# Kernel optimization log

Hardware: AMD Instinct MI355X
Metric: run time of the kernel (lower is better)

Reference implementation:

```python
import jax, jax.numpy as jnp
import numpy as np

N = 100000
E = 1600000
D_IN = 128
D_HID = 128
EPS = 1e-5  # BatchNorm eps


def gcn_conv(x, edge_index, W, b, num_nodes):
    # PyG GCNConv: h = x @ W; symmetric norm with self-loops; out = scatter_add + b
    h = x @ W  # [N, D_out]
    loops = jnp.arange(num_nodes, dtype=edge_index.dtype)
    src = jnp.concatenate([edge_index[0], loops])
    dst = jnp.concatenate([edge_index[1], loops])
    ones = jnp.ones(src.shape[0], dtype=h.dtype)
    deg = jax.ops.segment_sum(ones, dst, num_segments=num_nodes)  # in-degree incl. self-loop
    dinv = jnp.where(deg > 0, jax.lax.rsqrt(deg), 0.0)
    norm = dinv[src] * dinv[dst]  # [E+N]
    msg = h[src] * norm[:, None]  # [E+N, D_out]  (largest intermediate)
    out = jax.ops.segment_sum(msg, dst, num_segments=num_nodes)
    return out + b


def batchnorm(h, gamma, beta):
    # training-mode batch statistics over the node dimension (biased variance)
    mean = jnp.mean(h, axis=0)
    var = jnp.mean(jnp.square(h - mean), axis=0)
    return (h - mean) * jax.lax.rsqrt(var + EPS) * gamma + beta


def setup_inputs() -> dict:
    key = jax.random.key(0)
    ks = jax.random.split(key, 8)
    x = jax.random.normal(ks[0], (N, D_IN), dtype=jnp.float32)
    edge_index = jax.random.randint(ks[1], (2, E), 0, N, dtype=jnp.int64)
    s1 = 1.0 / np.sqrt(D_IN)
    s2 = 1.0 / np.sqrt(D_HID)
    W1 = jax.random.uniform(ks[2], (D_IN, D_HID), jnp.float32, -s1, s1)
    b1 = jnp.zeros((D_HID,), jnp.float32)
    g1 = jnp.ones((D_HID,), jnp.float32)
    be1 = jnp.zeros((D_HID,), jnp.float32)
    W2 = jax.random.uniform(ks[3], (D_HID, D_HID), jnp.float32, -s2, s2)
    b2 = jnp.zeros((D_HID,), jnp.float32)
    g2 = jnp.ones((D_HID,), jnp.float32)
    be2 = jnp.zeros((D_HID,), jnp.float32)
    Wl = jax.random.uniform(ks[4], (D_HID, 1), jnp.float32, -s2, s2)
    bl = jax.random.uniform(ks[5], (1,), jnp.float32, -s2, s2)
    return {"x": x, "edge_index": edge_index, "W1": W1, "b1": b1, "g1": g1,
            "be1": be1, "W2": W2, "b2": b2, "g2": g2, "be2": be2,
            "Wl": Wl, "bl": bl}


def reference(x, edge_index, W1, b1, g1, be1, W2, b2, g2, be2, Wl, bl):
    h = gcn_conv(x, edge_index, W1, b1, N)
    h = jax.nn.relu(batchnorm(h, g1, be1))
    # dropout is identity in eval/deterministic reference
    h = gcn_conv(h, edge_index, W2, b2, N)
    h = jax.nn.relu(batchnorm(h, g2, be2))
    h = jax.nn.relu(h @ Wl + bl)  # [N, 1]
    return jax.nn.sigmoid(h)
```

## Files before the change

### kernel.cpp

```cpp
#include <hip/hip_runtime.h>
#include <cstdint>
#include <cstddef>

typedef unsigned int uint;
typedef unsigned short ushort;
typedef __attribute__((ext_vector_type(8))) short bf16x8;
typedef __attribute__((ext_vector_type(4))) float f32x4;

#define CAP 4608

__device__ __forceinline__ ushort f2bf(float f) {
    uint b = __float_as_uint(f);
    return (ushort)((b + 0x7FFF + ((b >> 16) & 1)) >> 16);
}
__device__ __forceinline__ float bf_lo(uint u) { return __uint_as_float(u << 16); }
__device__ __forceinline__ float bf_hi(uint u) { return __uint_as_float(u & 0xFFFF0000u); }

__global__ __launch_bounds__(512) void k_sort(
        const int* __restrict__ src, const int* __restrict__ dst, int E, int chunk,
        int* __restrict__ bcur, uint* __restrict__ ebuf, int nbkt,
        const float* __restrict__ W1, const float* __restrict__ W2,
        ushort* __restrict__ WT1, ushort* __restrict__ WT2,
        float* __restrict__ sums) {
    __shared__ uint   ebuf_l[8192];
    __shared__ ushort bid_l[8192];
    __shared__ int    sh[512];
    __shared__ int    hist[512], histx[512], cur[512], goff[512];
    const int t   = threadIdx.x;
    const int blk = blockIdx.x;

    {
        int wi = blk * 512 + t;
        if (wi < 16384) {
            int nn = wi >> 7, k = wi & 127;
            WT1[wi] = f2bf(W1[k * 128 + nn]);
        } else if (wi < 32768) {
            int wj = wi - 16384, nn = wj >> 7, k = wj & 127;
            WT2[wj] = f2bf(W2[k * 128 + nn]);
        } else if (wi < 36864) {
            sums[wi - 32768] = 0.f;
        }
    }

    hist[t] = 0;
    __syncthreads();

    const int beg = blk * chunk;
    const int end = min(beg + chunk, E);
    for (int i = beg + t; i < end; i += 512)
        atomicAdd(&hist[dst[i] >> 8], 1);
    __syncthreads();

    const int c = (t < nbkt) ? hist[t] : 0;
    sh[t] = c;
    __syncthreads();
    #pragma unroll
    for (int o = 1; o < 512; o <<= 1) {
        int x = (t >= o) ? sh[t - o] : 0;
        __syncthreads();
        sh[t] += x;
        __syncthreads();
    }
    const int ex = sh[t] - c;
    histx[t] = ex;
    cur[t]   = ex;
    {
        int base = (c > 0 && t < nbkt) ? atomicAdd(&bcur[t], c) : 0;
        goff[t] = t * CAP + base - ex;
    }
    __syncthreads();

    for (int i = beg + t; i < end; i += 512) {
        int d = dst[i];
        int s = src[i];
        int b = d >> 8;
        int p = atomicAdd(&cur[b], 1);
        ebuf_l[p] = ((uint)(d & 255) << 17) | (uint)s;
        bid_l[p]  = (ushort)b;
    }
    __syncthreads();

    const int cntE = end - beg;
    for (int i = t; i < cntE; i += 512)
        ebuf[goff[bid_l[i]] + i] = ebuf_l[i];
}

__global__ __launch_bounds__(256) void k_bcsr(
        const uint* __restrict__ ebuf, const int* __restrict__ bcur,
        int n, float* __restrict__ dinv, int* __restrict__ offs,
        int* __restrict__ deg, int* __restrict__ csr) {
    __shared__ int fine[256], finex[256], fcur[256];
    const int b = blockIdx.x;
    const int t = threadIdx.x;
    const int ebeg = b * CAP;
    const int eend = ebeg + bcur[b];
    fine[t] = 0;
    __syncthreads();
    for (int i = ebeg + t; i < eend; i += 256)
        atomicAdd(&fine[ebuf[i] >> 17], 1);
    __syncthreads();
    const int node = b * 256 + t;
    if (node < n) {
        dinv[node] = rsqrtf((float)(fine[t] + 1));
        deg[node]  = fine[t];
    }
    int v = fine[t];
    finex[t] = v;
    __syncthreads();
    #pragma unroll
    for (int o = 1; o < 256; o <<= 1) {
        int x = (t >= o) ? finex[t - o] : 0;
        __syncthreads();
        finex[t] += x;
        __syncthreads();
    }
    const int ex = finex[t] - v;
    fcur[t] = ex;
    if (node < n) offs[node] = ebeg + ex;
    __syncthreads();
    for (int i = ebeg + t; i < eend; i += 256) {
        uint e = ebuf[i];
        int f = (int)(e >> 17);
        int p = atomicAdd(&fcur[f], 1);
        csr[ebeg + p] = (int)(e & 0x1FFFF);
    }
}

template <int LAYER>
__global__ __launch_bounds__(256) void k_gemm(
        const void* __restrict__ Av, const ushort* __restrict__ WT,
        const float* __restrict__ sums, const float* __restrict__ g,
        const float* __restrict__ be, const float* __restrict__ dinv,
        ushort* __restrict__ C, int n, float invn) {
    __shared__ ushort sWT[128 * 128];
    __shared__ float  ssl[256];
    const int tid  = threadIdx.x;
    const int lane = tid & 63;
    const int wid  = tid >> 6;
    const int m0   = blockIdx.x * 64 + wid * 16;
    const int lm   = lane & 15;
    const int lq   = lane >> 4;
    const int row  = m0 + lm;
    const bool rv  = row < n;

    float4 a0f[8];
    uint4  a1u[4];
    if (LAYER == 0) {
        const float* A = (const float*)Av;
        #pragma unroll
        for (int ks = 0; ks < 4; ks++) {
            const int kb = ks * 32 + lq * 8;
            if (rv) {
                a0f[2 * ks]     = *(const float4*)&A[(size_t)row * 128 + kb];
                a0f[2 * ks + 1] = *(const float4*)&A[(size_t)row * 128 + kb + 4];
            } else {
                a0f[2 * ks] = make_float4(0.f, 0.f, 0.f, 0.f);
                a0f[2 * ks + 1] = a0f[2 * ks];
            }
        }
    } else {
        const uint* A = (const uint*)Av;
        #pragma unroll
        for (int ks = 0; ks < 4; ks++) {
            const int kb = ks * 32 + lq * 8;
            a1u[ks] = rv ? *(const uint4*)&A[(size_t)row * 64 + kb / 2]
                         : make_uint4(0, 0, 0, 0);
        }
    }

    {
        const uint4* WT4 = (const uint4*)WT;
        char* sB = (char*)sWT;
        #pragma unroll
        for (int i = 0; i < 8; i++) {
            int idx  = tid + i * 256;
            uint4 v  = WT4[idx];
            int nrow = idx >> 4, j = idx & 15;
            int byte = (nrow * 256 + j * 16) ^ ((nrow & 7) << 4);
            *(uint4*)(sB + byte) = v;
        }
    }
    if (LAYER == 1 && tid < 128) {
        float s = 0.f, s2 = 0.f;
        #pragma unroll
        for (int b = 0; b < 8; b++) {
            s  += sums[b * 256 + tid];
            s2 += sums[b * 256 + 128 + tid];
        }
        float mean = s * invn;
        float var  = s2 * invn - mean * mean;
        float inv  = rsqrtf(var + 1e-5f);
        float sc   = g[tid] * inv;
        ssl[tid]       = sc;
        ssl[128 + tid] = be[tid] - mean * sc;
    }
    __syncthreads();

    f32x4 acc[8];
    #pragma unroll
    for (int i = 0; i < 8; i++) acc[i] = (f32x4){0.f, 0.f, 0.f, 0.f};

    const char* sB = (const char*)sWT;
    #pragma unroll
    for (int ks = 0; ks < 4; ks++) {
        const int kb = ks * 32 + lq * 8;
        bf16x8 af;
        if (LAYER == 0) {
            float4 v0 = a0f[2 * ks], v1 = a0f[2 * ks + 1];
            af[0] = (short)f2bf(v0.x); af[1] = (short)f2bf(v0.y);
            af[2] = (short)f2bf(v0.z); af[3] = (short)f2bf(v0.w);
            af[4] = (short)f2bf(v1.x); af[5] = (short)f2bf(v1.y);
            af[6] = (short)f2bf(v1.z); af[7] = (short)f2bf(v1.w);
        } else {
            uint4 u = a1u[ks];
            float4 sc0 = *(const float4*)&ssl[kb];
            float4 sc1 = *(const float4*)&ssl[kb + 4];
            float4 sh0 = *(const float4*)&ssl[128 + kb];
            float4 sh1 = *(const float4*)&ssl[128 + kb + 4];
            float f0 = fmaxf(fmaf(bf_lo(u.x), sc0.x, sh0.x), 0.f);
            float f1 = fmaxf(fmaf(bf_hi(u.x), sc0.y, sh0.y), 0.f);
            float f2 = fmaxf(fmaf(bf_lo(u.y), sc0.z, sh0.z), 0.f);
            float f3 = fmaxf(fmaf(bf_hi(u.y), sc0.w, sh0.w), 0.f);
            float f4 = fmaxf(fmaf(bf_lo(u.z), sc1.x, sh1.x), 0.f);
            float f5 = fmaxf(fmaf(bf_hi(u.z), sc1.y, sh1.y), 0.f);
            float f6 = fmaxf(fmaf(bf_lo(u.w), sc1.z, sh1.z), 0.f);
            float f7 = fmaxf(fmaf(bf_hi(u.w), sc1.w, sh1.w), 0.f);
            af[0] = (short)f2bf(f0); af[1] = (short)f2bf(f1);
            af[2] = (short)f2bf(f2); af[3] = (short)f2bf(f3);
            af[4] = (short)f2bf(f4); af[5] = (short)f2bf(f5);
            af[6] = (short)f2bf(f6); af[7] = (short)f2bf(f7);
        }
        #pragma unroll
        for (int nt = 0; nt < 8; nt++) {
            const int r    = nt * 16 + lm;
            const int byte = (r * 256 + ks * 64 + lq * 16) ^ ((r & 7) << 4);
            bf16x8 bfr = *(const bf16x8*)(sB + byte);
            acc[nt] = __builtin_amdgcn_mfma_f32_16x16x32_bf16(af, bfr, acc[nt], 0, 0, 0);
        }
    }

    const int orow0 = m0 + lq * 4;
    #pragma unroll
    for (int r = 0; r < 4; r++) {
        const int orow = orow0 + r;
        if (orow < n) {
            const float s = dinv[orow];
            #pragma unroll
            for (int nt = 0; nt < 8; nt++)
                C[(size_t)orow * 128 + nt * 16 + lm] = f2bf(acc[nt][r] * s);
        }
    }
}

__global__ __launch_bounds__(256) void k_gather(
        const uint* __restrict__ hs, const int* __restrict__ offs,
        const int* __restrict__ deg, const int* __restrict__ csr,
        const float* __restrict__ dinv, const float* __restrict__ bias,
        uint* __restrict__ out, float* __restrict__ sums_out, int n) {
    __shared__ float red[4][256];
    const int t = threadIdx.x;
    const int lane = t & 63;
    const int wid  = t >> 6;
    const int q  = lane & 15;
    const int eg = lane >> 4;
    const int wv = (blockIdx.x * 256 + t) >> 6;
    const int nw = gridDim.x * 4;
    const uint4* hs4 = (const uint4*)hs;
    const float4 b0 = *(const float4*)&bias[q * 8];
    const float4 b1 = *(const float4*)&bias[q * 8 + 4];

    float rs[8], rq[8];
    #pragma unroll
    for (int j = 0; j < 8; j++) { rs[j] = 0.f; rq[j] = 0.f; }

    for (int node = wv; node < n; node += nw) {
        const int beg = offs[node];
        const int end = beg + deg[node];

        float acc[8];
        if (eg == 0) {
            uint4 sv = hs4[(size_t)node * 16 + q];
            acc[0] = bf_lo(sv.x); acc[1] = bf_hi(sv.x);
            acc[2] = bf_lo(sv.y); acc[3] = bf_hi(sv.y);
            acc[4] = bf_lo(sv.z); acc[5] = bf_hi(sv.z);
            acc[6] = bf_lo(sv.w); acc[7] = bf_hi(sv.w);
        } else {
            #pragma unroll
            for (int j = 0; j < 8; j++) acc[j] = 0.f;
        }

        for (int e = beg + eg; e < end; e += 4) {
            const int s = csr[e];
            uint4 v = hs4[(size_t)s * 16 + q];
            acc[0] += bf_lo(v.x); acc[1] += bf_hi(v.x);
            acc[2] += bf_lo(v.y); acc[3] += bf_hi(v.y);
            acc[4] += bf_lo(v.z); acc[5] += bf_hi(v.z);
            acc[6] += bf_lo(v.w); acc[7] += bf_hi(v.w);
        }

        #pragma unroll
        for (int j = 0; j < 8; j++) {
            acc[j] += __shfl_xor(acc[j], 16);
            acc[j] += __shfl_xor(acc[j], 32);
        }

        if (eg == 0) {
            const float di = dinv[node];
            float o0 = fmaf(di, acc[0], b0.x), o1 = fmaf(di, acc[1], b0.y);
            float o2 = fmaf(di, acc[2], b0.z), o3 = fmaf(di, acc[3], b0.w);
            float o4 = fmaf(di, acc[4], b1.x), o5 = fmaf(di, acc[5], b1.y);
            float o6 = fmaf(di, acc[6], b1.z), o7 = fmaf(di, acc[7], b1.w);
            uint4 o;
            o.x = (uint)f2bf(o0) | ((uint)f2bf(o1) << 16);
            o.y = (uint)f2bf(o2) | ((uint)f2bf(o3) << 16);
            o.z = (uint)f2bf(o4) | ((uint)f2bf(o5) << 16);
            o.w = (uint)f2bf(o6) | ((uint)f2bf(o7) << 16);
            ((uint4*)out)[(size_t)node * 16 + q] = o;
            rs[0] += o0; rq[0] = fmaf(o0, o0, rq[0]);
            rs[1] += o1; rq[1] = fmaf(o1, o1, rq[1]);
            rs[2] += o2; rq[2] = fmaf(o2, o2, rq[2]);
            rs[3] += o3; rq[3] = fmaf(o3, o3, rq[3]);
            rs[4] += o4; rq[4] = fmaf(o4, o4, rq[4]);
            rs[5] += o5; rq[5] = fmaf(o5, o5, rq[5]);
            rs[6] += o6; rq[6] = fmaf(o6, o6, rq[6]);
            rs[7] += o7; rq[7] = fmaf(o7, o7, rq[7]);
        }
    }

    if (eg == 0) {
        #pragma unroll
        for (int j = 0; j < 8; j++) {
            red[wid][q * 8 + j]       = rs[j];
            red[wid][128 + q * 8 + j] = rq[j];
        }
    }
    __syncthreads();
    float v = red[0][t] + red[1][t] + red[2][t] + red[3][t];
    atomicAdd(&sums_out[(blockIdx.x & 7) * 256 + t], v);
}

__global__ __launch_bounds__(1024) void k_final(
        const uint* __restrict__ h, const float* __restrict__ sums,
        const float* __restrict__ g, const float* __restrict__ be,
        const float* __restrict__ Wl, const float* __restrict__ bl,
        float* __restrict__ out, int n, float invn) {
    __shared__ float ssl[256];
    const int t = threadIdx.x;
    if (t < 128) {
        float s = 0.f, s2 = 0.f;
        #pragma unroll
        for (int b = 0; b < 8; b++) {
            s  += sums[b * 256 + t];
            s2 += sums[b * 256 + 128 + t];
        }
        float mean = s * invn;
        float var  = s2 * invn - mean * mean;
        float inv  = rsqrtf(var + 1e-5f);
        float sc   = g[t] * inv;
        ssl[t]       = sc;
        ssl[128 + t] = be[t] - mean * sc;
    }
    __syncthreads();
    int node = (blockIdx.x * 1024 + t) >> 6;
    int lane = t & 63;
    if (node >= n) return;
    int c = lane * 2;
    uint v = h[(size_t)node * 64 + lane];
    float a0 = fmaxf(fmaf(bf_lo(v), ssl[c],     ssl[128 + c]),     0.f);
    float a1 = fmaxf(fmaf(bf_hi(v), ssl[c + 1], ssl[128 + c + 1]), 0.f);
    float p = a0 * Wl[c] + a1 * Wl[c + 1];
    #pragma unroll
    for (int o = 32; o; o >>= 1) p += __shfl_xor(p, o);
    if (lane == 0) {
        float z = fmaxf(p + bl[0], 0.f);
        out[node] = 1.f / (1.f + expf(-z));
    }
}

extern "C" void kernel_launch(void* const* d_in, const int* in_sizes, int n_in,
                              void* d_out, int out_size, void* d_ws, size_t ws_size,
                              hipStream_t stream) {
    const float* x   = (const float*)d_in[0];
    const int*   ei  = (const int*)d_in[1];
    const float* W1  = (const float*)d_in[2];
    const float* b1  = (const float*)d_in[3];
    const float* g1  = (const float*)d_in[4];
    const float* be1 = (const float*)d_in[5];
    const float* W2  = (const float*)d_in[6];
    const float* b2  = (const float*)d_in[7];
    const float* g2  = (const float*)d_in[8];
    const float* be2 = (const float*)d_in[9];
    const float* Wl  = (const float*)d_in[10];
    const float* bl  = (const float*)d_in[11];

    const int N = in_sizes[0] / 128;
    const int E = in_sizes[1] / 2;
    const int* src  = ei;
    const int* dstp = ei + E;

    const int NBKT  = (N + 255) >> 8;
    const int CHUNK = (E + 255) / 256;

    char* ws = (char*)d_ws;
    size_t off = 0;
    auto alloc = [&](size_t bytes) {
        void* p = ws + off;
        off += (bytes + 255) & ~(size_t)255;
        return p;
    };
    float*  dinv   = (float*) alloc((size_t)N * 4);
    int*    offs   = (int*)   alloc((size_t)N * 4);
    int*    deg    = (int*)   alloc((size_t)N * 4);
    int*    bcur   = (int*)   alloc((size_t)NBKT * 4);
    uint*   ebuf   = (uint*)  alloc((size_t)NBKT * CAP * 4);
    int*    csr    = (int*)   alloc((size_t)NBKT * CAP * 4);
    float*  sums   = (float*) alloc(16 * 256 * 4);
    ushort* WT1    = (ushort*)alloc(128 * 128 * 2);
    ushort* WT2    = (ushort*)alloc(128 * 128 * 2);
    ushort* hbuf   = (ushort*)alloc((size_t)N * 128 * 2);
    ushort* abuf   = (ushort*)alloc((size_t)N * 128 * 2);

    const float invn = 1.f / (float)N;

    hipMemsetAsync(bcur, 0, (size_t)NBKT * 4, stream);

    k_sort <<<256, 512, 0, stream>>>(src, dstp, E, CHUNK, bcur, ebuf, NBKT,
                                     W1, W2, WT1, WT2, sums);
    k_bcsr <<<NBKT, 256, 0, stream>>>(ebuf, bcur, N, dinv, offs, deg, csr);

    k_gemm<0> <<<(N + 63) / 64, 256, 0, stream>>>(x, WT1, nullptr, nullptr, nullptr, dinv, hbuf, N, invn);
    k_gather  <<<2048, 256, 0, stream>>>((const uint*)hbuf, offs, deg, csr, dinv, b1, (uint*)abuf, sums, N);

    k_gemm<1> <<<(N + 63) / 64, 256, 0, stream>>>(abuf, WT2, sums, g1, be1, dinv, hbuf, N, invn);
    k_gather  <<<2048, 256, 0, stream>>>((const uint*)hbuf, offs, deg, csr, dinv, b2, (uint*)abuf, sums + 2048, N);

    k_final<<<(N + 15) / 16, 1024, 0, stream>>>((const uint*)abuf, sums + 2048, g2, be2, Wl, bl, (float*)d_out, N, invn);
}
```

Baseline: 234.6 us.

## Run layer-1 GEMM concurrently with edge bucketing in one fused build kernel

The first-layer GEMM (x @ W1) now runs in extra blocks of the edge-sorting kernel, so it overlaps with edge bucketing. The dinv pre-scaling that layer 1 used to apply in its GEMM epilogue moves into the first gather, which multiplies each neighbour row by dinv[src] on the fly. This removes one kernel launch and the serial dependency of GEMM1 on the CSR build. In exchange the first gather does an extra dinv load and FMAs per edge, the fused kernel needs a large shared memory footprint, and GEMM1 stores results with scattered 2-byte writes.

```diff
diff --git a/kernel.cpp b/kernel.cpp
--- a/kernel.cpp
+++ b/kernel.cpp
@@ -16,73 +16,166 @@
 __device__ __forceinline__ float bf_lo(uint u) { return __uint_as_float(u << 16); }
 __device__ __forceinline__ float bf_hi(uint u) { return __uint_as_float(u & 0xFFFF0000u); }
 
-__global__ __launch_bounds__(512) void k_sort(
+__global__ __launch_bounds__(512) void k_build(
         const int* __restrict__ src, const int* __restrict__ dst, int E, int chunk,
         int* __restrict__ bcur, uint* __restrict__ ebuf, int nbkt,
         const float* __restrict__ W1, const float* __restrict__ W2,
-        ushort* __restrict__ WT1, ushort* __restrict__ WT2,
-        float* __restrict__ sums) {
-    __shared__ uint   ebuf_l[8192];
-    __shared__ ushort bid_l[8192];
-    __shared__ int    sh[512];
-    __shared__ int    hist[512], histx[512], cur[512], goff[512];
-    const int t   = threadIdx.x;
-    const int blk = blockIdx.x;
-
-    {
-        int wi = blk * 512 + t;
-        if (wi < 16384) {
-            int nn = wi >> 7, k = wi & 127;
-            WT1[wi] = f2bf(W1[k * 128 + nn]);
-        } else if (wi < 32768) {
-            int wj = wi - 16384, nn = wj >> 7, k = wj & 127;
-            WT2[wj] = f2bf(W2[k * 128 + nn]);
-        } else if (wi < 36864) {
-            sums[wi - 32768] = 0.f;
-        }
-    }
-
-    hist[t] = 0;
-    __syncthreads();
-
-    const int beg = blk * chunk;
-    const int end = min(beg + chunk, E);
-    for (int i = beg + t; i < end; i += 512)
-        atomicAdd(&hist[dst[i] >> 8], 1);
-    __syncthreads();
-
-    const int c = (t < nbkt) ? hist[t] : 0;
-    sh[t] = c;
-    __syncthreads();
-    #pragma unroll
-    for (int o = 1; o < 512; o <<= 1) {
-        int x = (t >= o) ? sh[t - o] : 0;
-        __syncthreads();
-        sh[t] += x;
-        __syncthreads();
-    }
-    const int ex = sh[t] - c;
-    histx[t] = ex;
-    cur[t]   = ex;
-    {
-        int base = (c > 0 && t < nbkt) ? atomicAdd(&bcur[t], c) : 0;
-        goff[t] = t * CAP + base - ex;
-    }
-    __syncthreads();
-
-    for (int i = beg + t; i < end; i += 512) {
-        int d = dst[i];
-        int s = src[i];
-        int b = d >> 8;
-        int p = atomicAdd(&cur[b], 1);
-        ebuf_l[p] = ((uint)(d & 255) << 17) | (uint)s;
-        bid_l[p]  = (ushort)b;
-    }
-    __syncthreads();
-
-    const int cntE = end - beg;
-    for (int i = t; i < cntE; i += 512)
-        ebuf[goff[bid_l[i]] + i] = ebuf_l[i];
+        ushort* __restrict__ WT2, float* __restrict__ sums,
+        const float* __restrict__ x, ushort* __restrict__ C, int n) {
+    __shared__ char smem[66560];
+    const int t = threadIdx.x;
+
+    if (blockIdx.x < 256) {
+        uint*   ebuf_l = (uint*)smem;
+        ushort* bid_l  = (ushort*)(smem + 32768);
+        int*    sh     = (int*)(smem + 49152);
+        int*    hist   = sh + 512;
+        int*    cur    = hist + 512;
+        int*    goff   = cur + 512;
+        const int blk = blockIdx.x;
+
+        {
+            int wi = blk * 512 + t;
+            if (wi < 16384) {
+                int nn = wi >> 7, k = wi & 127;
+                WT2[wi] = f2bf(W2[k * 128 + nn]);
+            } else if (wi < 20480) {
+                sums[wi - 16384] = 0.f;
+            }
+        }
+
+        hist[t] = 0;
+        __syncthreads();
+
+        const int beg = blk * chunk;
+        const int end = min(beg + chunk, E);
+        for (int i = beg + t; i < end; i += 512)
+            atomicAdd(&hist[dst[i] >> 8], 1);
+        __syncthreads();
+
+        const int c = (t < nbkt) ? hist[t] : 0;
+        sh[t] = c;
+        __syncthreads();
+        #pragma unroll
+        for (int o = 1; o < 512; o <<= 1) {
+            int v = (t >= o) ? sh[t - o] : 0;
+            __syncthreads();
+            sh[t] += v;
+            __syncthreads();
+        }
+        const int ex = sh[t] - c;
+        cur[t] = ex;
+        {
+            int base = (c > 0 && t < nbkt) ? atomicAdd(&bcur[t], c) : 0;
+            goff[t] = t * CAP + base - ex;
+        }
+        __syncthreads();
+
+        for (int i = beg + t; i < end; i += 512) {
+            int d = dst[i];
+            int s = src[i];
+            int b = d >> 8;
+            int p = atomicAdd(&cur[b], 1);
+            ebuf_l[p] = ((uint)(d & 255) << 17) | (uint)s;
+            bid_l[p]  = (ushort)b;
+        }
+        __syncthreads();
+
+        const int cntE = end - beg;
+        for (int i = t; i < cntE; i += 512)
+            ebuf[goff[bid_l[i]] + i] = ebuf_l[i];
+        return;
+    }
+
+    ushort* scratch = (ushort*)smem;
+    ushort* sWT     = (ushort*)(smem + 33792);
+    const int lane = t & 63;
+    const int wid  = t >> 6;
+    const int m0   = ((int)blockIdx.x - 256) * 128 + wid * 16;
+    const int lm   = lane & 15;
+    const int lq   = lane >> 4;
+    const int row  = m0 + lm;
+    const bool rv  = row < n;
+
+    float4 a0f[8];
+    #pragma unroll
+    for (int ks = 0; ks < 4; ks++) {
+        const int kb = ks * 32 + lq * 8;
+        if (rv) {
+            a0f[2 * ks]     = *(const float4*)&x[(size_t)row * 128 + kb];
+            a0f[2 * ks + 1] = *(const float4*)&x[(size_t)row * 128 + kb + 4];
+        } else {
+            a0f[2 * ks] = make_float4(0.f, 0.f, 0.f, 0.f);
+            a0f[2 * ks + 1] = a0f[2 * ks];
+        }
+    }
+
+    #pragma unroll
+    for (int i = 0; i < 8; i++) {
+        int idx = t + i * 512;
+        float4 w = ((const float4*)W1)[idx];
+        int k = idx >> 5, n0 = (idx & 31) * 4;
+        uint2 p;
+        p.x = (uint)f2bf(w.x) | ((uint)f2bf(w.y) << 16);
+        p.y = (uint)f2bf(w.z) | ((uint)f2bf(w.w) << 16);
+        *(uint2*)&scratch[k * 132 + n0] = p;
+    }
+    __syncthreads();
+
+    #pragma unroll
+    for (int i = 0; i < 4; i++) {
+        int oidx = t + i * 512;
+        int nn = oidx >> 4, k0 = (oidx & 15) * 8;
+        ushort s0 = scratch[(k0 + 0) * 132 + nn];
+        ushort s1 = scratch[(k0 + 1) * 132 + nn];
+        ushort s2 = scratch[(k0 + 2) * 132 + nn];
+        ushort s3 = scratch[(k0 + 3) * 132 + nn];
+        ushort s4 = scratch[(k0 + 4) * 132 + nn];
+        ushort s5 = scratch[(k0 + 5) * 132 + nn];
+        ushort s6 = scratch[(k0 + 6) * 132 + nn];
+        ushort s7 = scratch[(k0 + 7) * 132 + nn];
+        uint4 w;
+        w.x = (uint)s0 | ((uint)s1 << 16);
+        w.y = (uint)s2 | ((uint)s3 << 16);
+        w.z = (uint)s4 | ((uint)s5 << 16);
+        w.w = (uint)s6 | ((uint)s7 << 16);
+        int byte = (nn * 256 + k0 * 2) ^ ((nn & 7) << 4);
+        *(uint4*)((char*)sWT + byte) = w;
+    }
+    __syncthreads();
+
+    f32x4 acc[8];
+    #pragma unroll
+    for (int i = 0; i < 8; i++) acc[i] = (f32x4){0.f, 0.f, 0.f, 0.f};
+
+    const char* sB = (const char*)sWT;
+    #pragma unroll
+    for (int ks = 0; ks < 4; ks++) {
+        bf16x8 af;
+        float4 v0 = a0f[2 * ks], v1 = a0f[2 * ks + 1];
+        af[0] = (short)f2bf(v0.x); af[1] = (short)f2bf(v0.y);
+        af[2] = (short)f2bf(v0.z); af[3] = (short)f2bf(v0.w);
+        af[4] = (short)f2bf(v1.x); af[5] = (short)f2bf(v1.y);
+        af[6] = (short)f2bf(v1.z); af[7] = (short)f2bf(v1.w);
+        #pragma unroll
+        for (int nt = 0; nt < 8; nt++) {
+            const int r    = nt * 16 + lm;
+            const int byte = (r * 256 + ks * 64 + lq * 16) ^ ((r & 7) << 4);
+            bf16x8 bfr = *(const bf16x8*)(sB + byte);
+            acc[nt] = __builtin_amdgcn_mfma_f32_16x16x32_bf16(af, bfr, acc[nt], 0, 0, 0);
+        }
+    }
+
+    const int orow0 = m0 + lq * 4;
+    #pragma unroll
+    for (int r = 0; r < 4; r++) {
+        const int orow = orow0 + r;
+        if (orow < n) {
+            #pragma unroll
+            for (int nt = 0; nt < 8; nt++)
+                C[(size_t)orow * 128 + nt * 16 + lm] = f2bf(acc[nt][r]);
+        }
+    }
 }
 
 __global__ __launch_bounds__(256) void k_bcsr(
@@ -126,9 +219,8 @@
     }
 }
 
-template <int LAYER>
-__global__ __launch_bounds__(256) void k_gemm(
-        const void* __restrict__ Av, const ushort* __restrict__ WT,
+__global__ __launch_bounds__(256) void k_gemm1(
+        const uint* __restrict__ A, const ushort* __restrict__ WT,
         const float* __restrict__ sums, const float* __restrict__ g,
         const float* __restrict__ be, const float* __restrict__ dinv,
         ushort* __restrict__ C, int n, float invn) {
@@ -143,44 +235,27 @@
     const int row  = m0 + lm;
     const bool rv  = row < n;
 
-    float4 a0f[8];
-    uint4  a1u[4];
-    if (LAYER == 0) {
-        const float* A = (const float*)Av;
-        #pragma unroll
-        for (int ks = 0; ks < 4; ks++) {
-            const int kb = ks * 32 + lq * 8;
-            if (rv) {
-                a0f[2 * ks]     = *(const float4*)&A[(size_t)row * 128 + kb];
-                a0f[2 * ks + 1] = *(const float4*)&A[(size_t)row * 128 + kb + 4];
-            } else {
-                a0f[2 * ks] = make_float4(0.f, 0.f, 0.f, 0.f);
-                a0f[2 * ks + 1] = a0f[2 * ks];
-            }
-        }
-    } else {
-        const uint* A = (const uint*)Av;
-        #pragma unroll
-        for (int ks = 0; ks < 4; ks++) {
-            const int kb = ks * 32 + lq * 8;
-            a1u[ks] = rv ? *(const uint4*)&A[(size_t)row * 64 + kb / 2]
-                         : make_uint4(0, 0, 0, 0);
-        }
+    uint4 a1u[4];
+    #pragma unroll
+    for (int ks = 0; ks < 4; ks++) {
+        const int kb = ks * 32 + lq * 8;
+        a1u[ks] = rv ? *(const uint4*)&A[(size_t)row * 64 + kb / 2]
+                     : make_uint4(0, 0, 0, 0);
     }
 
     {
         const uint4* WT4 = (const uint4*)WT;
-        char* sB = (char*)sWT;
+        char* sBw = (char*)sWT;
         #pragma unroll
         for (int i = 0; i < 8; i++) {
             int idx  = tid + i * 256;
             uint4 v  = WT4[idx];
             int nrow = idx >> 4, j = idx & 15;
             int byte = (nrow * 256 + j * 16) ^ ((nrow & 7) << 4);
-            *(uint4*)(sB + byte) = v;
-        }
-    }
-    if (LAYER == 1 && tid < 128) {
+            *(uint4*)(sBw + byte) = v;
+        }
+    }
+    if (tid < 128) {
         float s = 0.f, s2 = 0.f;
         #pragma unroll
         for (int b = 0; b < 8; b++) {
@@ -204,32 +279,24 @@
     #pragma unroll
     for (int ks = 0; ks < 4; ks++) {
         const int kb = ks * 32 + lq * 8;
+        uint4 u = a1u[ks];
+        float4 sc0 = *(const float4*)&ssl[kb];
+        float4 sc1 = *(const float4*)&ssl[kb + 4];
+        float4 sh0 = *(const float4*)&ssl[128 + kb];
+        float4 sh1 = *(const float4*)&ssl[128 + kb + 4];
+        float f0 = fmaxf(fmaf(bf_lo(u.x), sc0.x, sh0.x), 0.f);
+        float f1 = fmaxf(fmaf(bf_hi(u.x), sc0.y, sh0.y), 0.f);
+        float f2 = fmaxf(fmaf(bf_lo(u.y), sc0.z, sh0.z), 0.f);
+        float f3 = fmaxf(fmaf(bf_hi(u.y), sc0.w, sh0.w), 0.f);
+        float f4 = fmaxf(fmaf(bf_lo(u.z), sc1.x, sh1.x), 0.f);
+        float f5 = fmaxf(fmaf(bf_hi(u.z), sc1.y, sh1.y), 0.f);
+        float f6 = fmaxf(fmaf(bf_lo(u.w), sc1.z, sh1.z), 0.f);
+        float f7 = fmaxf(fmaf(bf_hi(u.w), sc1.w, sh1.w), 0.f);
         bf16x8 af;
-        if (LAYER == 0) {
-            float4 v0 = a0f[2 * ks], v1 = a0f[2 * ks + 1];
-            af[0] = (short)f2bf(v0.x); af[1] = (short)f2bf(v0.y);
-            af[2] = (short)f2bf(v0.z); af[3] = (short)f2bf(v0.w);
-            af[4] = (short)f2bf(v1.x); af[5] = (short)f2bf(v1.y);
-            af[6] = (short)f2bf(v1.z); af[7] = (short)f2bf(v1.w);
-        } else {
-            uint4 u = a1u[ks];
-            float4 sc0 = *(const float4*)&ssl[kb];
-            float4 sc1 = *(const float4*)&ssl[kb + 4];
-            float4 sh0 = *(const float4*)&ssl[128 + kb];
-            float4 sh1 = *(const float4*)&ssl[128 + kb + 4];
-            float f0 = fmaxf(fmaf(bf_lo(u.x), sc0.x, sh0.x), 0.f);
-            float f1 = fmaxf(fmaf(bf_hi(u.x), sc0.y, sh0.y), 0.f);
-            float f2 = fmaxf(fmaf(bf_lo(u.y), sc0.z, sh0.z), 0.f);
-            float f3 = fmaxf(fmaf(bf_hi(u.y), sc0.w, sh0.w), 0.f);
-            float f4 = fmaxf(fmaf(bf_lo(u.z), sc1.x, sh1.x), 0.f);
-            float f5 = fmaxf(fmaf(bf_hi(u.z), sc1.y, sh1.y), 0.f);
-            float f6 = fmaxf(fmaf(bf_lo(u.w), sc1.z, sh1.z), 0.f);
-            float f7 = fmaxf(fmaf(bf_hi(u.w), sc1.w, sh1.w), 0.f);
-            af[0] = (short)f2bf(f0); af[1] = (short)f2bf(f1);
-            af[2] = (short)f2bf(f2); af[3] = (short)f2bf(f3);
-            af[4] = (short)f2bf(f4); af[5] = (short)f2bf(f5);
-            af[6] = (short)f2bf(f6); af[7] = (short)f2bf(f7);
-        }
+        af[0] = (short)f2bf(f0); af[1] = (short)f2bf(f1);
+        af[2] = (short)f2bf(f2); af[3] = (short)f2bf(f3);
+        af[4] = (short)f2bf(f4); af[5] = (short)f2bf(f5);
+        af[6] = (short)f2bf(f6); af[7] = (short)f2bf(f7);
         #pragma unroll
         for (int nt = 0; nt < 8; nt++) {
             const int r    = nt * 16 + lm;
@@ -252,6 +319,7 @@
     }
 }
 
+template <int PRE>
 __global__ __launch_bounds__(256) void k_gather(
         const uint* __restrict__ hs, const int* __restrict__ offs,
         const int* __restrict__ deg, const int* __restrict__ csr,
@@ -276,14 +344,22 @@
     for (int node = wv; node < n; node += nw) {
         const int beg = offs[node];
         const int end = beg + deg[node];
+        const float di = dinv[node];
 
         float acc[8];
         if (eg == 0) {
             uint4 sv = hs4[(size_t)node * 16 + q];
-            acc[0] = bf_lo(sv.x); acc[1] = bf_hi(sv.x);
-            acc[2] = bf_lo(sv.y); acc[3] = bf_hi(sv.y);
-            acc[4] = bf_lo(sv.z); acc[5] = bf_hi(sv.z);
-            acc[6] = bf_lo(sv.w); acc[7] = bf_hi(sv.w);
+            if (PRE) {
+                acc[0] = bf_lo(sv.x); acc[1] = bf_hi(sv.x);
+                acc[2] = bf_lo(sv.y); acc[3] = bf_hi(sv.y);
+                acc[4] = bf_lo(sv.z); acc[5] = bf_hi(sv.z);
+                acc[6] = bf_lo(sv.w); acc[7] = bf_hi(sv.w);
+            } else {
+                acc[0] = di * bf_lo(sv.x); acc[1] = di * bf_hi(sv.x);
+                acc[2] = di * bf_lo(sv.y); acc[3] = di * bf_hi(sv.y);
+                acc[4] = di * bf_lo(sv.z); acc[5] = di * bf_hi(sv.z);
+                acc[6] = di * bf_lo(sv.w); acc[7] = di * bf_hi(sv.w);
+            }
         } else {
             #pragma unroll
             for (int j = 0; j < 8; j++) acc[j] = 0.f;
@@ -292,10 +368,18 @@
         for (int e = beg + eg; e < end; e += 4) {
             const int s = csr[e];
             uint4 v = hs4[(size_t)s * 16 + q];
-            acc[0] += bf_lo(v.x); acc[1] += bf_hi(v.x);
-            acc[2] += bf_lo(v.y); acc[3] += bf_hi(v.y);
-            acc[4] += bf_lo(v.z); acc[5] += bf_hi(v.z);
-            acc[6] += bf_lo(v.w); acc[7] += bf_hi(v.w);
+            if (PRE) {
+                acc[0] += bf_lo(v.x); acc[1] += bf_hi(v.x);
+                acc[2] += bf_lo(v.y); acc[3] += bf_hi(v.y);
+                acc[4] += bf_lo(v.z); acc[5] += bf_hi(v.z);
+                acc[6] += bf_lo(v.w); acc[7] += bf_hi(v.w);
+            } else {
+                const float w = dinv[s];
+                acc[0] = fmaf(w, bf_lo(v.x), acc[0]); acc[1] = fmaf(w, bf_hi(v.x), acc[1]);
+                acc[2] = fmaf(w, bf_lo(v.y), acc[2]); acc[3] = fmaf(w, bf_hi(v.y), acc[3]);
+                acc[4] = fmaf(w, bf_lo(v.z), acc[4]); acc[5] = fmaf(w, bf_hi(v.z), acc[5]);
+                acc[6] = fmaf(w, bf_lo(v.w), acc[6]); acc[7] = fmaf(w, bf_hi(v.w), acc[7]);
+            }
         }
 
         #pragma unroll
@@ -305,7 +389,6 @@
         }
 
         if (eg == 0) {
-            const float di = dinv[node];
             float o0 = fmaf(di, acc[0], b0.x), o1 = fmaf(di, acc[1], b0.y);
             float o2 = fmaf(di, acc[2], b0.z), o3 = fmaf(di, acc[3], b0.w);
             float o4 = fmaf(di, acc[4], b1.x), o5 = fmaf(di, acc[5], b1.y);
@@ -400,6 +483,7 @@
 
     const int NBKT  = (N + 255) >> 8;
     const int CHUNK = (E + 255) / 256;
+    const int NG    = (N + 127) / 128;
 
     char* ws = (char*)d_ws;
     size_t off = 0;
@@ -415,7 +499,6 @@
     uint*   ebuf   = (uint*)  alloc((size_t)NBKT * CAP * 4);
     int*    csr    = (int*)   alloc((size_t)NBKT * CAP * 4);
     float*  sums   = (float*) alloc(16 * 256 * 4);
-    ushort* WT1    = (ushort*)alloc(128 * 128 * 2);
     ushort* WT2    = (ushort*)alloc(128 * 128 * 2);
     ushort* hbuf   = (ushort*)alloc((size_t)N * 128 * 2);
     ushort* abuf   = (ushort*)alloc((size_t)N * 128 * 2);
@@ -424,15 +507,14 @@
 
     hipMemsetAsync(bcur, 0, (size_t)NBKT * 4, stream);
 
-    k_sort <<<256, 512, 0, stream>>>(src, dstp, E, CHUNK, bcur, ebuf, NBKT,
-                                     W1, W2, WT1, WT2, sums);
-    k_bcsr <<<NBKT, 256, 0, stream>>>(ebuf, bcur, N, dinv, offs, deg, csr);
-
-    k_gemm<0> <<<(N + 63) / 64, 256, 0, stream>>>(x, WT1, nullptr, nullptr, nullptr, dinv, hbuf, N, invn);
-    k_gather  <<<2048, 256, 0, stream>>>((const uint*)hbuf, offs, deg, csr, dinv, b1, (uint*)abuf, sums, N);
-
-    k_gemm<1> <<<(N + 63) / 64, 256, 0, stream>>>(abuf, WT2, sums, g1, be1, dinv, hbuf, N, invn);
-    k_gather  <<<2048, 256, 0, stream>>>((const uint*)hbuf, offs, deg, csr, dinv, b2, (uint*)abuf, sums + 2048, N);
+    k_build <<<256 + NG, 512, 0, stream>>>(src, dstp, E, CHUNK, bcur, ebuf, NBKT,
+                                           W1, W2, WT2, sums, x, hbuf, N);
+    k_bcsr  <<<NBKT, 256, 0, stream>>>(ebuf, bcur, N, dinv, offs, deg, csr);
+
+    k_gather<0> <<<2048, 256, 0, stream>>>((const uint*)hbuf, offs, deg, csr, dinv, b1, (uint*)abuf, sums, N);
+
+    k_gemm1     <<<(N + 63) / 64, 256, 0, stream>>>((const uint*)abuf, WT2, sums, g1, be1, dinv, hbuf, N, invn);
+    k_gather<1> <<<2048, 256, 0, stream>>>((const uint*)hbuf, offs, deg, csr, dinv, b2, (uint*)abuf, sums + 2048, N);
 
     k_final<<<(N + 15) / 16, 1024, 0, stream>>>((const uint*)abuf, sums + 2048, g2, be2, Wl, bl, (float*)d_out, N, invn);
 }
```

Measured after the change: 231.9 us. Within noise of the previous version (-1.2%).
